# Kernel tuning notes

Measured on AMD Instinct MI355X. Metric: run time of the kernel, lower is better.

The kernel has to match this reference:

```python
import jax, jax.numpy as jnp
import numpy as np

IN_FEATURES = 4096
OUT_FEATURES = 4096
BLOCKSIZE = 64
FP4_CODEBOOK = np.array([0.0, 0.0052, 0.6667, 1.0, 0.3333, 0.5, 0.1667, 0.25,
                         0.0, -0.0052, -0.6667, -1.0, -0.3333, -0.5, -0.1667, -0.25],
                        dtype=np.float32)


def setup_inputs() -> dict:
    key = jax.random.key(0)
    k1, k2, k3, k4 = jax.random.split(key, 4)
    n_elements = OUT_FEATURES * IN_FEATURES
    n_blocks = n_elements // BLOCKSIZE
    x = jax.random.normal(k1, (4, 2048, IN_FEATURES), dtype=jnp.float32)
    weight_packed = jax.random.randint(k2, (n_elements // 2,), 0, 256, dtype=jnp.int32)
    scale = jax.random.uniform(k3, (n_blocks,), dtype=jnp.float32)
    bias = jax.random.normal(k4, (OUT_FEATURES,), dtype=jnp.float32)
    return {"x": x, "weight_packed": weight_packed, "scale": scale, "bias": bias}


def reference(x, weight_packed, scale, bias):
    codebook = jnp.asarray(FP4_CODEBOOK, dtype=x.dtype)
    # Unpack two 4-bit indices per byte: high nibble first, then low nibble.
    high = (weight_packed >> 4) & 15
    low = weight_packed & 15
    indices = jnp.stack([high, low], axis=1).reshape(-1)  # [n_elements]
    # LUT dequant + per-block scale broadcast.
    deq = codebook[indices].reshape(-1, BLOCKSIZE) * scale[:, None]  # [n_blocks, blocksize]
    weight = deq.reshape(OUT_FEATURES, IN_FEATURES)
    # F.linear(x, W, b) = x @ W.T + b
    return jnp.einsum('bsi,oi->bso', x, weight) + bias
```

## Files before the change

### kernel.cpp

```cpp
#include <hip/hip_runtime.h>
#include <stdint.h>
#include <stddef.h>

#define IN_F 4096
#define OUT_F 4096
#define M_TOT 8192

#define BM 128
#define BN 128
#define BK 64

#define BM2 256
#define BN2 256
#define BK2 64
#define NT2 (IN_F / BK2)

typedef __attribute__((ext_vector_type(8))) short short8;
typedef __attribute__((ext_vector_type(4))) float f32x4;
typedef __attribute__((ext_vector_type(4))) float float4v;
typedef __attribute__((ext_vector_type(4))) unsigned short u16x4;
typedef __attribute__((ext_vector_type(8))) unsigned short u16x8;
typedef unsigned short u16;

__constant__ float c_lut[16] = {
  0.0f, 0.0052f, 0.6667f, 1.0f, 0.3333f, 0.5f, 0.1667f, 0.25f,
  0.0f, -0.0052f, -0.6667f, -1.0f, -0.3333f, -0.5f, -0.1667f, -0.25f
};

__device__ __forceinline__ u16 f2bf(float f) {
  unsigned int x = __float_as_uint(f);
  x += 0x7fffu + ((x >> 16) & 1u);
  return (u16)(x >> 16);
}

__device__ __forceinline__ void gload_lds16(const u16* g, u16* lds) {
  __builtin_amdgcn_global_load_lds(
      (const __attribute__((address_space(1))) unsigned int*)g,
      (__attribute__((address_space(3))) unsigned int*)lds, 16, 0, 0);
}

#define BARRIER() do { asm volatile("" ::: "memory"); \
                       __builtin_amdgcn_s_barrier();  \
                       asm volatile("" ::: "memory"); } while (0)
#define LGKM0() asm volatile("s_waitcnt lgkmcnt(0)" ::: "memory")

__global__ __launch_bounds__(256) void k_prep(const float* __restrict__ x,
                                              u16* __restrict__ a,
                                              const int* __restrict__ wp,
                                              const float* __restrict__ scale,
                                              u16* __restrict__ b) {
  if (blockIdx.x < 512) {
    __shared__ float lut[16];
    if (threadIdx.x < 16) lut[threadIdx.x] = c_lut[threadIdx.x];
    __syncthreads();
    const int ng = (OUT_F * IN_F / 2) / 4;
    const int stride = 512 * 256;
    for (int t = blockIdx.x * 256 + threadIdx.x; t < ng; t += stride) {
      int4 p = ((const int4*)wp)[t];
      float s = scale[t >> 3];
      int by[4] = {p.x, p.y, p.z, p.w};
      u16x8 o;
#pragma unroll
      for (int q = 0; q < 4; ++q) {
        o[2 * q]     = f2bf(lut[(by[q] >> 4) & 15] * s);
        o[2 * q + 1] = f2bf(lut[by[q] & 15] * s);
      }
      ((u16x8*)b)[t] = o;
    }
  } else {
    const int n8 = (M_TOT * IN_F) / 8;
    const int stride = 4096 * 256;
    for (int t = (blockIdx.x - 512) * 256 + threadIdx.x; t < n8; t += stride) {
      float4v f0 = ((const float4v*)x)[2 * t];
      float4v f1 = ((const float4v*)x)[2 * t + 1];
      u16x8 o;
      o[0] = f2bf(f0.x); o[1] = f2bf(f0.y); o[2] = f2bf(f0.z); o[3] = f2bf(f0.w);
      o[4] = f2bf(f1.x); o[5] = f2bf(f1.y); o[6] = f2bf(f1.z); o[7] = f2bf(f1.w);
      ((u16x8*)a)[t] = o;
    }
  }
}


__device__ __forceinline__ void stage_b_round(const u16* __restrict__ B, u16* dst,
                                              int nBase, int kt, int r,
                                              int wave, int srow, int scol) {
  const int r0 = r * 64 + wave * 8;
  gload_lds16(B + (size_t)(nBase + r0 + srow) * IN_F + kt + scol, dst + r0 * BK2);
}

__device__ __forceinline__ void stage_a_round(const u16* __restrict__ A, u16* dst,
                                              int mBase, int kt, int r,
                                              int wave, int srow, int scol) {
  const int r0 = (wave & 3) * 8 + (wave >> 2) * 128 + r * 32;
  gload_lds16(A + (size_t)(mBase + r0 + srow) * IN_F + kt + scol, dst + r0 * BK2);
}

__device__ __forceinline__ void read_b_all(const u16* Bs_c, int bBase, int co0, int co1,
                                           short8 b[4][2]) {
#pragma unroll
  for (int jj = 0; jj < 4; ++jj) {
    const int ro = bBase + jj * (16 * BK2);
    b[jj][0] = *(const short8*)&Bs_c[ro + co0];
    b[jj][1] = *(const short8*)&Bs_c[ro + co1];
  }
}

__device__ __forceinline__ void read_a_pair(const u16* As_c, int aBase, int co0, int co1,
                                            short8 a[2][2], int p) {
#pragma unroll
  for (int ii = 0; ii < 2; ++ii) {
    const int ro = aBase + (p * 2 + ii) * (16 * BK2);
    a[ii][0] = *(const short8*)&As_c[ro + co0];
    a[ii][1] = *(const short8*)&As_c[ro + co1];
  }
}

__device__ __forceinline__ void mma_pair(f32x4 acc[8][4], const short8 a[2][2],
                                         const short8 b[4][2], int p) {
#pragma unroll
  for (int k2 = 0; k2 < 2; ++k2)
#pragma unroll
    for (int ii = 0; ii < 2; ++ii)
#pragma unroll
      for (int jj = 0; jj < 4; ++jj)
        acc[p * 2 + ii][jj] = __builtin_amdgcn_mfma_f32_16x16x32_bf16(
            a[ii][k2], b[jj][k2], acc[p * 2 + ii][jj], 0, 0, 0);
}

__global__ __launch_bounds__(512, 2) void k_gemm256(const u16* __restrict__ A,
                                                    const u16* __restrict__ B,
                                                    const float* __restrict__ bias,
                                                    float* __restrict__ C) {
  __shared__ u16 As[2][BM2 * BK2];
  __shared__ u16 Bs[2][BN2 * BK2];

  const int tid  = threadIdx.x;
  const int lane = tid & 63;
  const int wave = tid >> 6;

  const int bid   = blockIdx.x;
  const int xcd   = bid & 7;
  const int k     = bid >> 3;
  const int tileM = (xcd >> 1) * 8 + (k >> 3);
  const int tileN = (xcd & 1) * 8 + (k & 7);
  const int mBase = tileM * BM2;
  const int nBase = tileN * BN2;

  const int wm = (wave >> 2) * 128;
  const int wn = (wave & 3) * 64;

  const int srow = lane >> 3;
  const int scol = ((lane & 7) ^ srow) * 8;

  const int frow = lane & 15;
  const int fx   = frow & 7;
  const int cq   = lane >> 4;
  const int co0  = ((cq ^ fx) << 3);
  const int co1  = (((4 + cq) ^ fx) << 3);
  const int aBase = (wm + frow) * BK2;
  const int bBase = (wn + frow) * BK2;

  f32x4 acc[8][4] = {};
  short8 a[2][2], b[4][2];

#define SB(dst, t, r) stage_b_round(B, dst, nBase, (t) * BK2, r, wave, srow, scol)
#define SA(dst, t, r) stage_a_round(A, dst, mBase, (t) * BK2, r, wave, srow, scol)

  SB(Bs[0], 0, 0); SB(Bs[0], 0, 1); SB(Bs[0], 0, 2); SB(Bs[0], 0, 3);
  SA(As[0], 0, 0); SA(As[0], 0, 1); SA(As[0], 0, 2); SA(As[0], 0, 3);
  SB(Bs[1], 1, 0); SB(Bs[1], 1, 1); SA(As[1], 1, 0);
  SB(Bs[1], 1, 2); SB(Bs[1], 1, 3); SA(As[1], 1, 1);
  SA(As[1], 1, 2);
  asm volatile("s_waitcnt vmcnt(7)" ::: "memory");
  BARRIER();
  read_b_all(Bs[0], bBase, co0, co1, b);
  read_a_pair(As[0], aBase, co0, co1, a, 0);

  for (int t = 0; t < NT2; ++t) {
    const int c = t & 1;
    u16* AsC = As[c];
    u16* BsC = Bs[c];
    u16* AsO = As[c ^ 1];
    u16* BsO = Bs[c ^ 1];

    if (t + 1 < NT2) SA(AsO, t + 1, 3);
    LGKM0();
    __builtin_amdgcn_s_setprio(1);
    mma_pair(acc, a, b, 0);
    __builtin_amdgcn_s_setprio(0);
    read_a_pair(AsC, aBase, co0, co1, a, 1);
    BARRIER();

    if (t + 2 < NT2) { SB(BsC, t + 2, 0); SB(BsC, t + 2, 1); SA(AsC, t + 2, 0); }
    LGKM0();
    __builtin_amdgcn_s_setprio(1);
    mma_pair(acc, a, b, 1);
    __builtin_amdgcn_s_setprio(0);
    read_a_pair(AsC, aBase, co0, co1, a, 2);
    BARRIER();

    if (t + 2 < NT2) { SB(BsC, t + 2, 2); SB(BsC, t + 2, 3); SA(AsC, t + 2, 1); }
    LGKM0();
    __builtin_amdgcn_s_setprio(1);
    mma_pair(acc, a, b, 2);
    __builtin_amdgcn_s_setprio(0);
    read_a_pair(AsC, aBase, co0, co1, a, 3);
    BARRIER();

    if (t + 2 < NT2) SA(AsC, t + 2, 2);
    LGKM0();
    __builtin_amdgcn_s_setprio(1);
    mma_pair(acc, a, b, 3);
    __builtin_amdgcn_s_setprio(0);
    if (t + 1 < NT2) {
      if (t < NT2 - 2) asm volatile("s_waitcnt vmcnt(7)" ::: "memory");
      else             asm volatile("s_waitcnt vmcnt(0)" ::: "memory");
      read_b_all(BsO, bBase, co0, co1, b);
      read_a_pair(AsO, aBase, co0, co1, a, 0);
    }
    BARRIER();
  }

#undef SB
#undef SA

  const int ccol = lane & 15;
  const int crow = (lane >> 4) * 4;
#pragma unroll
  for (int j = 0; j < 4; ++j) {
    const int col = nBase + wn + j * 16 + ccol;
    const float bv = bias[col];
#pragma unroll
    for (int i = 0; i < 8; ++i) {
      const size_t rb = (size_t)(mBase + wm + i * 16 + crow) * OUT_F + col;
#pragma unroll
      for (int tt = 0; tt < 4; ++tt)
        C[rb + (size_t)tt * OUT_F] = acc[i][j][tt] + bv;
    }
  }
}

__global__ __launch_bounds__(256) void k_gemm_fused(const float* __restrict__ X,
                                                    const int* __restrict__ WP,
                                                    const float* __restrict__ scale,
                                                    const float* __restrict__ bias,
                                                    float* __restrict__ C) {
  __shared__ u16 As[BM * BK];
  __shared__ u16 Bs[BN * BK];
  __shared__ float lut[16];
  const int tid = threadIdx.x;
  if (tid < 16) lut[tid] = c_lut[tid];
  const int lane = tid & 63;
  const int wave = tid >> 6;
  const int mBase = blockIdx.y * BM;
  const int nBase = blockIdx.x * BN;
  const int wm = (wave >> 1) * 64;
  const int wn = (wave & 1) * 64;
  const int frow = lane & 15;
  const int fx   = lane & 7;
  const int cq   = lane >> 4;
  f32x4 acc[4][4] = {};
  __syncthreads();

  for (int kt = 0; kt < IN_F; kt += BK) {
#pragma unroll
    for (int i = 0; i < 8; ++i) {
      const int g = tid + i * 256;
      const int r = g >> 4, c = (g & 15) * 4;
      float4v f = *(const float4v*)&X[(size_t)(mBase + r) * IN_F + kt + c];
      u16x4 o;
      o.x = f2bf(f.x); o.y = f2bf(f.y); o.z = f2bf(f.z); o.w = f2bf(f.w);
      *(u16x4*)&As[r * BK + ((((c >> 3) ^ (r & 7)) << 3) | (c & 7))] = o;
    }
#pragma unroll
    for (int i = 0; i < 4; ++i) {
      const int g = tid + i * 256;
      const int r = g >> 3, c4 = (g & 7) * 4;
      int4 p = *(const int4*)&WP[(size_t)(nBase + r) * (IN_F / 2) + (kt >> 1) + c4];
      const float s = scale[(nBase + r) * 64 + (kt >> 6)];
      int by[4] = {p.x, p.y, p.z, p.w};
      u16x8 o;
#pragma unroll
      for (int q = 0; q < 4; ++q) {
        o[2 * q]     = f2bf(lut[(by[q] >> 4) & 15] * s);
        o[2 * q + 1] = f2bf(lut[by[q] & 15] * s);
      }
      *(u16x8*)&Bs[r * BK + (((g & 7) ^ (r & 7)) << 3)] = o;
    }
    __syncthreads();
#pragma unroll
    for (int ks = 0; ks < BK; ks += 32) {
      const int co = (((ks >> 3) + cq) ^ fx) << 3;
      short8 a[4], b[4];
#pragma unroll
      for (int i = 0; i < 4; ++i)
        a[i] = *(const short8*)&As[(wm + i * 16 + frow) * BK + co];
#pragma unroll
      for (int j = 0; j < 4; ++j)
        b[j] = *(const short8*)&Bs[(wn + j * 16 + frow) * BK + co];
#pragma unroll
      for (int i = 0; i < 4; ++i)
#pragma unroll
        for (int j = 0; j < 4; ++j)
          acc[i][j] = __builtin_amdgcn_mfma_f32_16x16x32_bf16(a[i], b[j], acc[i][j], 0, 0, 0);
    }
    __syncthreads();
  }

  const int ccol = lane & 15;
  const int crow = (lane >> 4) * 4;
#pragma unroll
  for (int j = 0; j < 4; ++j) {
    const int col = nBase + wn + j * 16 + ccol;
    const float bv = bias[col];
#pragma unroll
    for (int i = 0; i < 4; ++i) {
      const size_t rb = (size_t)(mBase + wm + i * 16 + crow) * OUT_F + col;
#pragma unroll
      for (int t = 0; t < 4; ++t)
        C[rb + (size_t)t * OUT_F] = acc[i][j][t] + bv;
    }
  }
}

extern "C" void kernel_launch(void* const* d_in, const int* in_sizes, int n_in,
                              void* d_out, int out_size, void* d_ws, size_t ws_size,
                              hipStream_t stream) {
  const float* x  = (const float*)d_in[0];
  const int*   wp = (const int*)d_in[1];
  const float* sc = (const float*)d_in[2];
  const float* bi = (const float*)d_in[3];
  float* out = (float*)d_out;

  const size_t bBytes = (size_t)OUT_F * IN_F * 2;
  const size_t aBytes = (size_t)M_TOT * IN_F * 2;

  if (ws_size >= aBytes + bBytes) {
    u16* B = (u16*)d_ws;
    u16* A = (u16*)((char*)d_ws + bBytes);
    k_prep<<<4608, 256, 0, stream>>>(x, A, wp, sc, B);
    k_gemm256<<<(M_TOT / BM2) * (OUT_F / BN2), 512, 0, stream>>>(A, B, bi, out);
  } else {
    dim3 grid(OUT_F / BN, M_TOT / BM);
    k_gemm_fused<<<grid, 256, 0, stream>>>(x, wp, sc, bi, out);
  }
}
```

Before: 502.4 us.

## Restructure GEMM main loop into quadrant MFMA schedule with finer waitcnts

Reorganizes the 256x256 GEMM inner loop so each wave computes four 4x2 quadrants of MFMAs instead of four 2x4 row pairs. A and B fragments are double-buffered in registers (aC/aN, b0/b1), and the global-to-LDS staging order is changed to a half/k split. Partial lgkmcnt/vmcnt waits with sched_barriers replace full lgkmcnt(0) waits, so LDS reads and global loads can overlap more MFMA work. The cost is more live registers and tighter hand-tuned wait counts, which could break correctness or occupancy if miscounted.

```diff
diff --git a/kernel.cpp b/kernel.cpp
--- a/kernel.cpp
+++ b/kernel.cpp
@@ -42,7 +42,9 @@
 #define BARRIER() do { asm volatile("" ::: "memory"); \
                        __builtin_amdgcn_s_barrier();  \
                        asm volatile("" ::: "memory"); } while (0)
-#define LGKM0() asm volatile("s_waitcnt lgkmcnt(0)" ::: "memory")
+#define LGW(n) do { asm volatile("s_waitcnt lgkmcnt(" #n ")" ::: "memory"); \
+                    __builtin_amdgcn_sched_barrier(0); } while (0)
+#define VMW(n) asm volatile("s_waitcnt vmcnt(" #n ")" ::: "memory")
 
 __global__ __launch_bounds__(256) void k_prep(const float* __restrict__ x,
                                               u16* __restrict__ a,
@@ -82,50 +84,47 @@
 }
 
 
-__device__ __forceinline__ void stage_b_round(const u16* __restrict__ B, u16* dst,
-                                              int nBase, int kt, int r,
-                                              int wave, int srow, int scol) {
-  const int r0 = r * 64 + wave * 8;
+__device__ __forceinline__ void st_b(const u16* __restrict__ B, u16* dst,
+                                     int nBase, int kt, int h, int k,
+                                     int wave, int srow, int scol) {
+  const int r0 = 64 * (wave >> 1) + 32 * h + 16 * k + 8 * (wave & 1);
   gload_lds16(B + (size_t)(nBase + r0 + srow) * IN_F + kt + scol, dst + r0 * BK2);
 }
-
-__device__ __forceinline__ void stage_a_round(const u16* __restrict__ A, u16* dst,
-                                              int mBase, int kt, int r,
-                                              int wave, int srow, int scol) {
-  const int r0 = (wave & 3) * 8 + (wave >> 2) * 128 + r * 32;
+__device__ __forceinline__ void st_a(const u16* __restrict__ A, u16* dst,
+                                     int mBase, int kt, int h, int k,
+                                     int wave, int srow, int scol) {
+  const int r0 = 128 * (wave >> 2) + 64 * h + 32 * k + 8 * (wave & 3);
   gload_lds16(A + (size_t)(mBase + r0 + srow) * IN_F + kt + scol, dst + r0 * BK2);
 }
 
-__device__ __forceinline__ void read_b_all(const u16* Bs_c, int bBase, int co0, int co1,
-                                           short8 b[4][2]) {
-#pragma unroll
-  for (int jj = 0; jj < 4; ++jj) {
-    const int ro = bBase + jj * (16 * BK2);
-    b[jj][0] = *(const short8*)&Bs_c[ro + co0];
-    b[jj][1] = *(const short8*)&Bs_c[ro + co1];
-  }
-}
-
-__device__ __forceinline__ void read_a_pair(const u16* As_c, int aBase, int co0, int co1,
-                                            short8 a[2][2], int p) {
-#pragma unroll
-  for (int ii = 0; ii < 2; ++ii) {
-    const int ro = aBase + (p * 2 + ii) * (16 * BK2);
-    a[ii][0] = *(const short8*)&As_c[ro + co0];
-    a[ii][1] = *(const short8*)&As_c[ro + co1];
-  }
-}
-
-__device__ __forceinline__ void mma_pair(f32x4 acc[8][4], const short8 a[2][2],
-                                         const short8 b[4][2], int p) {
+__device__ __forceinline__ void rd_b(short8 d[2][2], const u16* Bs_c, int bBase,
+                                     int co0, int co1, int h) {
+#pragma unroll
+  for (int jj = 0; jj < 2; ++jj) {
+    const int ro = bBase + (h * 2 + jj) * (16 * BK2);
+    d[jj][0] = *(const short8*)&Bs_c[ro + co0];
+    d[jj][1] = *(const short8*)&Bs_c[ro + co1];
+  }
+}
+__device__ __forceinline__ void rd_a(short8 d[4][2], const u16* As_c, int aBase,
+                                     int co0, int co1, int h) {
+#pragma unroll
+  for (int ii = 0; ii < 4; ++ii) {
+    const int ro = aBase + (h * 4 + ii) * (16 * BK2);
+    d[ii][0] = *(const short8*)&As_c[ro + co0];
+    d[ii][1] = *(const short8*)&As_c[ro + co1];
+  }
+}
+__device__ __forceinline__ void mma8(f32x4 acc[8][4], const short8 a[4][2],
+                                     const short8 b[2][2], int i0, int j0) {
 #pragma unroll
   for (int k2 = 0; k2 < 2; ++k2)
 #pragma unroll
-    for (int ii = 0; ii < 2; ++ii)
-#pragma unroll
-      for (int jj = 0; jj < 4; ++jj)
-        acc[p * 2 + ii][jj] = __builtin_amdgcn_mfma_f32_16x16x32_bf16(
-            a[ii][k2], b[jj][k2], acc[p * 2 + ii][jj], 0, 0, 0);
+    for (int ii = 0; ii < 4; ++ii)
+#pragma unroll
+      for (int jj = 0; jj < 2; ++jj)
+        acc[i0 + ii][j0 + jj] = __builtin_amdgcn_mfma_f32_16x16x32_bf16(
+            a[ii][k2], b[jj][k2], acc[i0 + ii][j0 + jj], 0, 0, 0);
 }
 
 __global__ __launch_bounds__(512, 2) void k_gemm256(const u16* __restrict__ A,
@@ -141,9 +140,9 @@
 
   const int bid   = blockIdx.x;
   const int xcd   = bid & 7;
-  const int k     = bid >> 3;
-  const int tileM = (xcd >> 1) * 8 + (k >> 3);
-  const int tileN = (xcd & 1) * 8 + (k & 7);
+  const int kk    = bid >> 3;
+  const int tileM = (xcd >> 1) * 8 + (kk >> 3);
+  const int tileN = (xcd & 1) * 8 + (kk & 7);
   const int mBase = tileM * BM2;
   const int nBase = tileN * BN2;
 
@@ -162,68 +161,74 @@
   const int bBase = (wn + frow) * BK2;
 
   f32x4 acc[8][4] = {};
-  short8 a[2][2], b[4][2];
-
-#define SB(dst, t, r) stage_b_round(B, dst, nBase, (t) * BK2, r, wave, srow, scol)
-#define SA(dst, t, r) stage_a_round(A, dst, mBase, (t) * BK2, r, wave, srow, scol)
-
-  SB(Bs[0], 0, 0); SB(Bs[0], 0, 1); SB(Bs[0], 0, 2); SB(Bs[0], 0, 3);
-  SA(As[0], 0, 0); SA(As[0], 0, 1); SA(As[0], 0, 2); SA(As[0], 0, 3);
-  SB(Bs[1], 1, 0); SB(Bs[1], 1, 1); SA(As[1], 1, 0);
-  SB(Bs[1], 1, 2); SB(Bs[1], 1, 3); SA(As[1], 1, 1);
-  SA(As[1], 1, 2);
-  asm volatile("s_waitcnt vmcnt(7)" ::: "memory");
+  short8 aC[4][2], aN[4][2], b0[2][2], b1[2][2];
+
+  st_b(B, Bs[0], nBase, 0, 0, 0, wave, srow, scol);
+  st_b(B, Bs[0], nBase, 0, 0, 1, wave, srow, scol);
+  st_b(B, Bs[0], nBase, 0, 1, 0, wave, srow, scol);
+  st_b(B, Bs[0], nBase, 0, 1, 1, wave, srow, scol);
+  st_a(A, As[0], mBase, 0, 0, 0, wave, srow, scol);
+  st_a(A, As[0], mBase, 0, 0, 1, wave, srow, scol);
+  st_a(A, As[0], mBase, 0, 1, 0, wave, srow, scol);
+  st_a(A, As[0], mBase, 0, 1, 1, wave, srow, scol);
+  st_b(B, Bs[1], nBase, BK2, 0, 0, wave, srow, scol);
+  st_b(B, Bs[1], nBase, BK2, 0, 1, wave, srow, scol);
+  st_a(A, As[1], mBase, BK2, 0, 0, wave, srow, scol);
+  st_a(A, As[1], mBase, BK2, 0, 1, wave, srow, scol);
+  st_b(B, Bs[1], nBase, BK2, 1, 0, wave, srow, scol);
+  st_b(B, Bs[1], nBase, BK2, 1, 1, wave, srow, scol);
+  VMW(6);
   BARRIER();
-  read_b_all(Bs[0], bBase, co0, co1, b);
-  read_a_pair(As[0], aBase, co0, co1, a, 0);
+  rd_a(aC, As[0], aBase, co0, co1, 0);
 
   for (int t = 0; t < NT2; ++t) {
     const int c = t & 1;
     u16* AsC = As[c];
     u16* BsC = Bs[c];
     u16* AsO = As[c ^ 1];
-    u16* BsO = Bs[c ^ 1];
-
-    if (t + 1 < NT2) SA(AsO, t + 1, 3);
-    LGKM0();
+
+    if (t < NT2 - 1) { VMW(6); } else { VMW(0); }
+    rd_b(b0, BsC, bBase, co0, co1, 0);
+    __builtin_amdgcn_sched_barrier(0);
+    rd_b(b1, BsC, bBase, co0, co1, 1);
+    if (t + 1 < NT2) st_a(A, AsO, mBase, (t + 1) * BK2, 1, 0, wave, srow, scol);
+    BARRIER();
+    LGW(4);
     __builtin_amdgcn_s_setprio(1);
-    mma_pair(acc, a, b, 0);
+    mma8(acc, aC, b0, 0, 0);
     __builtin_amdgcn_s_setprio(0);
-    read_a_pair(AsC, aBase, co0, co1, a, 1);
+
+    rd_a(aN, AsC, aBase, co0, co1, 1);
+    if (t + 1 < NT2) st_a(A, AsO, mBase, (t + 1) * BK2, 1, 1, wave, srow, scol);
     BARRIER();
-
-    if (t + 2 < NT2) { SB(BsC, t + 2, 0); SB(BsC, t + 2, 1); SA(AsC, t + 2, 0); }
-    LGKM0();
+    LGW(8);
     __builtin_amdgcn_s_setprio(1);
-    mma_pair(acc, a, b, 1);
+    mma8(acc, aC, b1, 0, 2);
     __builtin_amdgcn_s_setprio(0);
-    read_a_pair(AsC, aBase, co0, co1, a, 2);
+
+    VMW(2);
+    if (t + 2 < NT2) {
+      st_b(B, BsC, nBase, (t + 2) * BK2, 0, 0, wave, srow, scol);
+      st_b(B, BsC, nBase, (t + 2) * BK2, 0, 1, wave, srow, scol);
+      st_a(A, AsC, mBase, (t + 2) * BK2, 0, 0, wave, srow, scol);
+    }
     BARRIER();
-
-    if (t + 2 < NT2) { SB(BsC, t + 2, 2); SB(BsC, t + 2, 3); SA(AsC, t + 2, 1); }
-    LGKM0();
+    LGW(0);
     __builtin_amdgcn_s_setprio(1);
-    mma_pair(acc, a, b, 2);
+    mma8(acc, aN, b1, 4, 2);
     __builtin_amdgcn_s_setprio(0);
-    read_a_pair(AsC, aBase, co0, co1, a, 3);
+
+    if (t + 1 < NT2) rd_a(aC, AsO, aBase, co0, co1, 0);
+    if (t + 2 < NT2) {
+      st_a(A, AsC, mBase, (t + 2) * BK2, 0, 1, wave, srow, scol);
+      st_b(B, BsC, nBase, (t + 2) * BK2, 1, 0, wave, srow, scol);
+      st_b(B, BsC, nBase, (t + 2) * BK2, 1, 1, wave, srow, scol);
+    }
     BARRIER();
-
-    if (t + 2 < NT2) SA(AsC, t + 2, 2);
-    LGKM0();
     __builtin_amdgcn_s_setprio(1);
-    mma_pair(acc, a, b, 3);
+    mma8(acc, aN, b0, 4, 0);
     __builtin_amdgcn_s_setprio(0);
-    if (t + 1 < NT2) {
-      if (t < NT2 - 2) asm volatile("s_waitcnt vmcnt(7)" ::: "memory");
-      else             asm volatile("s_waitcnt vmcnt(0)" ::: "memory");
-      read_b_all(BsO, bBase, co0, co1, b);
-      read_a_pair(AsO, aBase, co0, co1, a, 0);
-    }
-    BARRIER();
-  }
-
-#undef SB
-#undef SA
+  }
 
   const int ccol = lane & 15;
   const int crow = (lane >> 4) * 4;
```

New measurement: 483.7 us. 1.04x faster.
